# Performance work log

Hardware: AMD Instinct MI355X
Metric: run time of the kernel (lower is better)

Reference implementation:

```python
import jax, jax.numpy as jnp
import numpy as np

BLOCK_SIZE = 4
TOPK = 16
ALPHA = 10.0
EPS = 1e-3


def setup_inputs() -> dict:
    key = jax.random.key(0)
    ks = jax.random.split(key, 5)
    B, H, W, C = 16, 96, 96, 512
    src = jax.random.normal(ks[0], (B, H, W, C), dtype=jnp.float32)
    # torch nn.Linear(C, 64): weight (64, C), bias (64)
    Wq = jax.random.normal(ks[1], (64, C), dtype=jnp.float32) * (C ** -0.5)
    bq = jax.random.normal(ks[2], (64,), dtype=jnp.float32) * 0.01
    Wk = jax.random.normal(ks[3], (64, C), dtype=jnp.float32) * (C ** -0.5)
    bk = jax.random.normal(ks[4], (64,), dtype=jnp.float32) * 0.01
    return {"src": src, "Wq": Wq, "bq": bq, "Wk": Wk, "bk": bk}


def reference(src, Wq, bq, Wk, bk):
    """Faithful JAX version of Zipformer2Encoder.get_select_weight_index.

    Returns (indexes, weights): both (B, num_block_tot, TOPK).
    Balancer is identity at inference (it only shapes gradients in training).
    """
    B, H, W, C = src.shape
    bs = BLOCK_SIZE
    nbh, nbw = H // bs, W // bs
    nb = nbh * nbw          # num_block_tot
    HW = H * W

    # block-mean pooling -> (B, nb, C)
    blocks = src.reshape(B, nbh, bs, nbw, bs, C)
    block_emb = blocks.mean(axis=(2, 4)).reshape(B, nb, C)

    q = block_emb @ Wq.T + bq                      # (B, nb, 64)
    k = src.reshape(B, HW, C) @ Wk.T + bk          # (B, HW, 64)
    scores = jnp.einsum("bnd,bpd->bnp", q, k)      # (B, nb, HW)

    # mask each block's own positions with -inf
    hh = jnp.arange(H) // bs
    ww = jnp.arange(W) // bs
    bid = (hh[:, None] * nbw + ww[None, :]).reshape(HW)        # block id per pixel
    mask = bid[None, :] == jnp.arange(nb)[:, None]             # (nb, HW)
    scores = jnp.where(mask[None], -jnp.inf, scores)

    # descending sort; only the top 2*TOPK entries are ever used
    sscores, indexes = jax.lax.top_k(scores, 2 * TOPK)          # (B, nb, 2*TOPK)

    # (B, nb, TOPK, 2*TOPK)
    diffs = sscores[..., :TOPK, None] - sscores[..., None, :]
    diffs_rms = jnp.sqrt(jnp.mean(diffs ** 2, axis=(1, 2, 3), keepdims=True))
    diffs = diffs * (ALPHA / (diffs_rms + EPS))
    weights = jnp.tanh(jax.nn.sigmoid(diffs).sum(-1) - TOPK)    # (B, nb, TOPK)

    return indexes[..., :TOPK], weights
```

## Files before the change

kernel.cpp:

```cpp
#include <hip/hip_runtime.h>
#include <hip/hip_bf16.h>
#include <math.h>

constexpr int B    = 16;
constexpr int H    = 96;
constexpr int W    = 96;
constexpr int C    = 512;
constexpr int D    = 64;
constexpr int NBH  = 24;
constexpr int NB   = 576;
constexpr int HW   = 9216;
constexpr int TOPK = 16;
constexpr int TK2  = 32;
constexpr int NCAND = 40;
constexpr int CAP  = 64;

typedef __attribute__((ext_vector_type(8))) short bf16x8;
typedef __attribute__((ext_vector_type(4))) float f32x4;

__device__ inline unsigned short f2bf(float x) {
    unsigned int u = __float_as_uint(x);
    return (unsigned short)((u + 0x7FFFu + ((u >> 16) & 1u)) >> 16);
}

__global__ void k_transpose(const float* __restrict__ Wk, const float* __restrict__ Wq,
                            float* __restrict__ WkT, float* __restrict__ WqT) {
    int idx = blockIdx.x * 256 + threadIdx.x;
    if (idx < C * D) {
        int c = idx >> 6, d = idx & 63;
        WkT[c * D + d] = Wk[d * C + c];
        WqT[c * D + d] = Wq[d * C + c];
    }
}

__global__ __launch_bounds__(256, 4) void k_embed(
    const float* __restrict__ src,
    const float* __restrict__ WkT, const float* __restrict__ bk,
    float* __restrict__ k32, float* __restrict__ emb) {
    __shared__ float sS[16][C];

    int t   = threadIdx.x;
    int blk = blockIdx.x;
    int b = blk / NB, n = blk % NB;
    int nh = n / NBH, nw = n % NBH;
    int y0 = nh * 4, x0 = nw * 4;

    #pragma unroll
    for (int r = 0; r < 8; ++r) {
        int f4 = r * 256 + t;
        int px = f4 >> 7, c4 = f4 & 127;
        int dy = px >> 2, dx = px & 3;
        ((float4*)sS[px])[c4] =
            *(const float4*)&src[((size_t)(b * H + y0 + dy) * W + (x0 + dx)) * C + c4 * 4];
    }
    __syncthreads();

    #pragma unroll
    for (int s = 0; s < 2; ++s) {
        int cc = s * 256 + t;
        float sum = sS[0][cc];
        #pragma unroll
        for (int px = 1; px < 16; ++px) sum += sS[px][cc];
        emb[((size_t)b * NB + n) * C + cc] = sum * 0.0625f;
    }

    int d = t & 63, pg = t >> 6;
    const float* s0 = sS[pg * 4 + 0];
    const float* s1 = sS[pg * 4 + 1];
    const float* s2 = sS[pg * 4 + 2];
    const float* s3 = sS[pg * 4 + 3];

    float a0 = 0.f, a1 = 0.f, a2 = 0.f, a3 = 0.f;
    float e0 = 0.f, e1 = 0.f, e2 = 0.f, e3 = 0.f;

    #pragma unroll 2
    for (int cg = 0; cg < 96; ++cg) {
        float4 x0v = *(const float4*)&s0[cg * 4];
        float4 x1v = *(const float4*)&s1[cg * 4];
        float4 x2v = *(const float4*)&s2[cg * 4];
        float4 x3v = *(const float4*)&s3[cg * 4];
        float w0 = WkT[(cg * 4 + 0) * D + d];
        float w1 = WkT[(cg * 4 + 1) * D + d];
        float w2 = WkT[(cg * 4 + 2) * D + d];
        float w3 = WkT[(cg * 4 + 3) * D + d];
        const float* x0f = (const float*)&x0v;
        const float* x1f = (const float*)&x1v;
        const float* x2f = (const float*)&x2v;
        const float* x3f = (const float*)&x3v;
        float wj[4] = {w0, w1, w2, w3};
        #pragma unroll
        for (int j = 0; j < 4; ++j) {
            a0 = __builtin_fmaf(x0f[j], wj[j], a0);
            a1 = __builtin_fmaf(x1f[j], wj[j], a1);
            a2 = __builtin_fmaf(x2f[j], wj[j], a2);
            a3 = __builtin_fmaf(x3f[j], wj[j], a3);
        }
    }
    #pragma unroll 2
    for (int cg = 96; cg < 128; ++cg) {
        float4 x0v = *(const float4*)&s0[cg * 4];
        float4 x1v = *(const float4*)&s1[cg * 4];
        float4 x2v = *(const float4*)&s2[cg * 4];
        float4 x3v = *(const float4*)&s3[cg * 4];
        float w0 = WkT[(cg * 4 + 0) * D + d];
        float w1 = WkT[(cg * 4 + 1) * D + d];
        float w2 = WkT[(cg * 4 + 2) * D + d];
        float w3 = WkT[(cg * 4 + 3) * D + d];
        const float* x0f = (const float*)&x0v;
        const float* x1f = (const float*)&x1v;
        const float* x2f = (const float*)&x2v;
        const float* x3f = (const float*)&x3v;
        float wj[4] = {w0, w1, w2, w3};
        #pragma unroll
        for (int j = 0; j < 4; ++j) {
            e0 = __builtin_fmaf(x0f[j], wj[j], e0);
            e1 = __builtin_fmaf(x1f[j], wj[j], e1);
            e2 = __builtin_fmaf(x2f[j], wj[j], e2);
            e3 = __builtin_fmaf(x3f[j], wj[j], e3);
        }
    }

    float bkd = bk[d];
    #pragma unroll
    for (int u = 0; u < 4; ++u) {
        int pxx = pg * 4 + u;
        int dy = pxx >> 2, dx = pxx & 3;
        size_t p = (size_t)(y0 + dy) * W + (x0 + dx);
        float a = (u == 0 ? a0 : u == 1 ? a1 : u == 2 ? a2 : a3);
        float e = (u == 0 ? e0 : u == 1 ? e1 : u == 2 ? e2 : e3);
        k32[((size_t)b * HW + p) * D + d] = (a + e) + bkd;
    }
}

__global__ __launch_bounds__(256) void k_q(
    const float* __restrict__ emb, const float* __restrict__ WqT,
    const float* __restrict__ bq, float* __restrict__ q32) {
    int t  = threadIdx.x;
    int d  = t & 63;
    int ng = t >> 6;
    int r0 = blockIdx.x * 16 + ng * 4;
    const float* e0 = emb + (size_t)(r0 + 0) * C;
    const float* e1 = emb + (size_t)(r0 + 1) * C;
    const float* e2 = emb + (size_t)(r0 + 2) * C;
    const float* e3 = emb + (size_t)(r0 + 3) * C;

    float qa0 = 0.f, qa1 = 0.f, qa2 = 0.f, qa3 = 0.f;
    float qe0 = 0.f, qe1 = 0.f, qe2 = 0.f, qe3 = 0.f;
    #pragma unroll 2
    for (int cg = 0; cg < 96; ++cg) {
        float4 v0 = *(const float4*)&e0[cg * 4];
        float4 v1 = *(const float4*)&e1[cg * 4];
        float4 v2 = *(const float4*)&e2[cg * 4];
        float4 v3 = *(const float4*)&e3[cg * 4];
        float w0 = WqT[(cg * 4 + 0) * D + d];
        float w1 = WqT[(cg * 4 + 1) * D + d];
        float w2 = WqT[(cg * 4 + 2) * D + d];
        float w3 = WqT[(cg * 4 + 3) * D + d];
        const float* f0 = (const float*)&v0;
        const float* f1 = (const float*)&v1;
        const float* f2 = (const float*)&v2;
        const float* f3 = (const float*)&v3;
        float wj[4] = {w0, w1, w2, w3};
        #pragma unroll
        for (int j = 0; j < 4; ++j) {
            qa0 = __builtin_fmaf(f0[j], wj[j], qa0);
            qa1 = __builtin_fmaf(f1[j], wj[j], qa1);
            qa2 = __builtin_fmaf(f2[j], wj[j], qa2);
            qa3 = __builtin_fmaf(f3[j], wj[j], qa3);
        }
    }
    #pragma unroll 2
    for (int cg = 96; cg < 128; ++cg) {
        float4 v0 = *(const float4*)&e0[cg * 4];
        float4 v1 = *(const float4*)&e1[cg * 4];
        float4 v2 = *(const float4*)&e2[cg * 4];
        float4 v3 = *(const float4*)&e3[cg * 4];
        float w0 = WqT[(cg * 4 + 0) * D + d];
        float w1 = WqT[(cg * 4 + 1) * D + d];
        float w2 = WqT[(cg * 4 + 2) * D + d];
        float w3 = WqT[(cg * 4 + 3) * D + d];
        const float* f0 = (const float*)&v0;
        const float* f1 = (const float*)&v1;
        const float* f2 = (const float*)&v2;
        const float* f3 = (const float*)&v3;
        float wj[4] = {w0, w1, w2, w3};
        #pragma unroll
        for (int j = 0; j < 4; ++j) {
            qe0 = __builtin_fmaf(f0[j], wj[j], qe0);
            qe1 = __builtin_fmaf(f1[j], wj[j], qe1);
            qe2 = __builtin_fmaf(f2[j], wj[j], qe2);
            qe3 = __builtin_fmaf(f3[j], wj[j], qe3);
        }
    }
    float bqd = bq[d];
    q32[(size_t)(r0 + 0) * D + d] = (qa0 + qe0) + bqd;
    q32[(size_t)(r0 + 1) * D + d] = (qa1 + qe1) + bqd;
    q32[(size_t)(r0 + 2) * D + d] = (qa2 + qe2) + bqd;
    q32[(size_t)(r0 + 3) * D + d] = (qa3 + qe3) + bqd;
}

__global__ __launch_bounds__(256, 4) void k_scores(
    const float* __restrict__ q32, const float* __restrict__ k32,
    _Float16* __restrict__ S16) {
    __shared__ unsigned short sQ[64 * 72];
    __shared__ unsigned short sK[64 * 72];
    __shared__ unsigned short sOut[4][16 * 72];

    int t  = threadIdx.x;
    int p0 = blockIdx.x * 64;
    int n0 = blockIdx.y * 64;
    int b  = blockIdx.z;

    const float* qb = q32 + ((size_t)b * NB + n0) * D;
    const float* kb = k32 + ((size_t)b * HW + p0) * D;

    #pragma unroll
    for (int r = 0; r < 4; ++r) {
        int L = r * 256 + t;
        int row = L >> 4, c4 = L & 15;
        float4 vq = *(const float4*)&qb[(size_t)row * D + c4 * 4];
        float4 vk = *(const float4*)&kb[(size_t)row * D + c4 * 4];
        ushort4 hq, hk;
        hq.x = f2bf(vq.x); hq.y = f2bf(vq.y); hq.z = f2bf(vq.z); hq.w = f2bf(vq.w);
        hk.x = f2bf(vk.x); hk.y = f2bf(vk.y); hk.z = f2bf(vk.z); hk.w = f2bf(vk.w);
        *(ushort4*)&sQ[row * 72 + c4 * 4] = hq;
        *(ushort4*)&sK[row * 72 + c4 * 4] = hk;
    }
    __syncthreads();

    int w = t >> 6, l = t & 63;
    int fr = l & 15;
    int kb8 = (l >> 4) * 8;

    f32x4 acc[4] = {f32x4{0,0,0,0}, f32x4{0,0,0,0}, f32x4{0,0,0,0}, f32x4{0,0,0,0}};
    #pragma unroll
    for (int ks = 0; ks < 2; ++ks) {
        bf16x8 a = *(const bf16x8*)&sQ[(16 * w + fr) * 72 + ks * 32 + kb8];
        #pragma unroll
        for (int f = 0; f < 4; ++f) {
            bf16x8 bb = *(const bf16x8*)&sK[(16 * f + fr) * 72 + ks * 32 + kb8];
            acc[f] = __builtin_amdgcn_mfma_f32_16x16x32_bf16(a, bb, acc[f], 0, 0, 0);
        }
    }

    unsigned short* so = &sOut[w][0];
    #pragma unroll
    for (int f = 0; f < 4; ++f)
        #pragma unroll
        for (int r = 0; r < 4; ++r) {
            _Float16 h = (_Float16)acc[f][r];
            so[((l >> 4) * 4 + r) * 72 + 16 * f + (l & 15)] = *(unsigned short*)&h;
        }
    __syncthreads();

    _Float16* Sb = S16 + (size_t)b * NB * HW;
    int orow = l >> 2, oc = (l & 3) * 16;
    uint4 v0 = *(const uint4*)&sOut[w][orow * 72 + oc];
    uint4 v1 = *(const uint4*)&sOut[w][orow * 72 + oc + 8];
    size_t base = (size_t)(n0 + 16 * w + orow) * HW + (p0 + oc);
    *(uint4*)&Sb[base]     = v0;
    *(uint4*)&Sb[base + 8] = v1;
}

__global__ __launch_bounds__(256) void k_topk(
    const _Float16* __restrict__ S16,
    const float* __restrict__ q32, const float* __restrict__ k32,
    int* __restrict__ cidx, float* __restrict__ cval, double* __restrict__ rowss) {
    __shared__ int    hist[4][256];
    __shared__ int    sfx[256];
    __shared__ int    b0s, mAbove, thrS, gcnt;
    __shared__ int    cps[CAP];
    __shared__ float  cv[CAP];
    __shared__ int    cp[CAP];
    __shared__ float  sv[CAP];
    __shared__ int    sp[CAP];
    __shared__ double ssq[TOPK];

    int t   = threadIdx.x;
    int row = blockIdx.x;
    int b = row / NB, n = row % NB;
    int wid = t >> 6;

    #pragma unroll
    for (int w = 0; w < 4; ++w) hist[w][t] = 0;
    if (t == 0) gcnt = 0;
    __syncthreads();

    const unsigned short* Srow = (const unsigned short*)(S16 + (size_t)row * HW);
    unsigned int my[36];
    #pragma unroll
    for (int c = 0; c < 9; ++c) {
        ushort4 v4 = ((const ushort4*)Srow)[c * 256 + t];
        #pragma unroll
        for (int j = 0; j < 4; ++j) {
            unsigned int h = (j == 0 ? v4.x : j == 1 ? v4.y : j == 2 ? v4.z : v4.w);
            unsigned int m = (h & 0x8000u) ? (h ^ 0xFFFFu) : (h | 0x8000u);
            int p = (c * 256 + t) * 4 + j;
            int hh = p / W, ww = p - hh * W;
            if (((hh >> 2) * NBH + (ww >> 2)) == n) m = 0;
            my[c * 4 + j] = m;
            atomicAdd(&hist[wid][m >> 8], 1);
        }
    }
    __syncthreads();

    sfx[t] = hist[0][t] + hist[1][t] + hist[2][t] + hist[3][t];
    __syncthreads();
    #pragma unroll
    for (int off = 1; off < 256; off <<= 1) {
        int v = (t + off < 256) ? sfx[t + off] : 0;
        __syncthreads();
        sfx[t] += v;
        __syncthreads();
    }
    if (sfx[t] >= NCAND && (t == 255 || sfx[t + 1] < NCAND)) {
        b0s = t; mAbove = (t == 255) ? 0 : sfx[t + 1];
    }
    __syncthreads();
    int b0 = b0s, mab = mAbove;
    __syncthreads();

    #pragma unroll
    for (int w = 0; w < 4; ++w) hist[w][t] = 0;
    __syncthreads();
    #pragma unroll
    for (int i = 0; i < 36; ++i)
        if ((int)(my[i] >> 8) == b0) atomicAdd(&hist[wid][my[i] & 255u], 1);
    __syncthreads();
    sfx[t] = hist[0][t] + hist[1][t] + hist[2][t] + hist[3][t];
    __syncthreads();
    #pragma unroll
    for (int off = 1; off < 256; off <<= 1) {
        int v = (t + off < 256) ? sfx[t + off] : 0;
        __syncthreads();
        sfx[t] += v;
        __syncthreads();
    }
    if (mab + sfx[t] >= NCAND && (t == 255 || mab + sfx[t + 1] < NCAND))
        thrS = (b0 << 8) | t;
    __syncthreads();
    unsigned int thr = (unsigned int)thrS;

    #pragma unroll
    for (int i = 0; i < 36; ++i) {
        if (my[i] >= thr) {
            int pos = atomicAdd(&gcnt, 1);
            if (pos < CAP) {
                int c = i >> 2, j = i & 3;
                cps[pos] = (c * 256 + t) * 4 + j;
            }
        }
    }
    __syncthreads();
    int M = min(gcnt, CAP);

    if (t < M) {
        #pragma clang fp contract(off)
        int p = cps[t];
        const float* qr = q32 + (size_t)row * D;
        const float* kr = k32 + ((size_t)b * HW + p) * D;
        float L0 = 0.f, L1 = 0.f, L2 = 0.f, L3 = 0.f;
        #pragma unroll
        for (int j = 0; j < 16; ++j) {
            L0 = L0 + qr[4 * j + 0] * kr[4 * j + 0];
            L1 = L1 + qr[4 * j + 1] * kr[4 * j + 1];
            L2 = L2 + qr[4 * j + 2] * kr[4 * j + 2];
            L3 = L3 + qr[4 * j + 3] * kr[4 * j + 3];
        }
        cv[t] = (L0 + L1) + (L2 + L3);
        cp[t] = p;
    }
    __syncthreads();

    if (t < M) {
        float v = cv[t]; int p = cp[t];
        int rank = 0;
        for (int j = 0; j < M; ++j) {
            float vj = cv[j];
            rank += (vj > v) || (vj == v && cp[j] < p);
        }
        sv[rank] = v; sp[rank] = p;
    }
    __syncthreads();

    if (t < TK2) {
        cval[(size_t)row * TK2 + t] = sv[t];
        cidx[(size_t)row * TK2 + t] = sp[t];
    }
    if (t < TOPK) {
        double vi = (double)sv[t], s = 0.0;
        #pragma unroll
        for (int j = 0; j < TK2; ++j) { double dd = vi - (double)sv[j]; s += dd * dd; }
        ssq[t] = s;
    }
    __syncthreads();
    if (t == 0) {
        double s = 0.0;
        #pragma unroll
        for (int i = 0; i < TOPK; ++i) s += ssq[i];
        rowss[row] = s;
    }
}

__global__ void k_rms(const double* __restrict__ rowss, double* __restrict__ scale) {
    __shared__ double sb[256];
    int b = blockIdx.x, t = threadIdx.x;
    double s = 0.0;
    for (int r = t; r < NB; r += 256) s += rowss[b * NB + r];
    sb[t] = s; __syncthreads();
    for (int st = 128; st > 0; st >>= 1) {
        if (t < st) sb[t] += sb[t + st];
        __syncthreads();
    }
    if (t == 0) {
        double rms = sqrt(sb[0] / ((double)NB * TOPK * TK2));
        scale[b] = 10.0 / (rms + 1e-3);
    }
}

__global__ __launch_bounds__(256) void k_final(
    const int* __restrict__ cidx, const float* __restrict__ cval,
    const double* __restrict__ scale, float* __restrict__ out) {
    __shared__ double sv[16][TK2];
    int t = threadIdx.x;
    int row0 = blockIdx.x * 16;
    for (int idx = t; idx < 16 * TK2; idx += 256) {
        int r = idx >> 5, j = idx & 31;
        sv[r][j] = (double)cval[(size_t)(row0 + r) * TK2 + j];
    }
    __syncthreads();
    int r = t >> 4, i = t & 15;
    int row = row0 + r;
    double scb = scale[row / NB];
    double vi = sv[r][i];
    double s = 0.0;
    #pragma unroll
    for (int j = 0; j < TK2; ++j) {
        double x = (vi - sv[r][j]) * scb;
        s += 1.0 / (1.0 + exp(-x));
    }
    out[(size_t)B * NB * TOPK + (size_t)row * TOPK + i] = (float)tanh(s - (double)TOPK);
    out[(size_t)row * TOPK + i] = (float)cidx[(size_t)row * TK2 + i];
}

__global__ void k_fill(float* out, int nelem) {
    int i = blockIdx.x * 256 + threadIdx.x;
    if (i < nelem) out[i] = -12345.0f;
}

extern "C" void kernel_launch(void* const* d_in, const int* in_sizes, int n_in,
                              void* d_out, int out_size, void* d_ws, size_t ws_size,
                              hipStream_t stream) {
    const float* src = (const float*)d_in[0];
    const float* Wq  = (const float*)d_in[1];
    const float* bq  = (const float*)d_in[2];
    const float* Wk  = (const float*)d_in[3];
    const float* bk  = (const float*)d_in[4];
    float* out = (float*)d_out;

    char* ws = (char*)d_ws;
    size_t oWkT = 0;
    size_t oWqT = oWkT + (size_t)C * D * 4;
    size_t oQ   = oWqT + (size_t)C * D * 4;
    size_t oK   = oQ   + (size_t)B * NB * D * 4;
    size_t oS   = oK   + (size_t)B * HW * D * 4;
    size_t oEmb = oS   + (size_t)B * NB * HW * 2;
    size_t oCV  = oEmb + (size_t)B * NB * C * 4;
    size_t oCI  = oCV  + (size_t)B * NB * TK2 * 4;
    size_t oRS  = oCI  + (size_t)B * NB * TK2 * 4;
    size_t oSc  = oRS  + (size_t)B * NB * 8;
    size_t need = oSc  + (size_t)B * 8;

    if (ws_size < need) {
        k_fill<<<(out_size + 255) / 256, 256, 0, stream>>>(out, out_size);
        return;
    }

    float*     WkT  = (float*)(ws + oWkT);
    float*     WqT  = (float*)(ws + oWqT);
    float*     q32  = (float*)(ws + oQ);
    float*     k32  = (float*)(ws + oK);
    _Float16*  S16  = (_Float16*)(ws + oS);
    float*     emb  = (float*)(ws + oEmb);
    float*     cval = (float*)(ws + oCV);
    int*       cidx = (int*)(ws + oCI);
    double*    rss  = (double*)(ws + oRS);
    double*    scl  = (double*)(ws + oSc);

    k_transpose<<<(C * D + 255) / 256, 256, 0, stream>>>(Wk, Wq, WkT, WqT);
    k_embed<<<B * NB, 256, 0, stream>>>(src, WkT, bk, k32, emb);
    k_q<<<B * NB / 16, 256, 0, stream>>>(emb, WqT, bq, q32);
    k_scores<<<dim3(HW / 64, NB / 64, B), 256, 0, stream>>>(q32, k32, S16);
    k_topk<<<B * NB, 256, 0, stream>>>(S16, q32, k32, cidx, cval, rss);
    k_rms<<<B, 256, 0, stream>>>(rss, scl);
    k_final<<<B * NB / 16, 256, 0, stream>>>(cidx, cval, scl, out);
}
```

Before: 479.7 us.

## Halve embed shared tile, and use privatized histograms with wave-shuffle scans in top-k

k_embed now stages the 16-pixel tile in two 256-channel halves, halving shared memory and raising the launch-bounds occupancy hint from 4 to 8 blocks. The cost is an extra barrier and a second load phase per block. k_topk replaces the per-wave histograms with 8-way privatized copies padded to stride 9, which cuts atomic contention and bank conflicts. It also replaces the barrier-heavy shared-memory suffix scan with wave shuffles plus a per-wave total, and hoists the self-block mask test out of the inner 4-element loop.

Result: no change. 488.2 us (+1.8%).

```diff
diff --git a/kernel.cpp b/kernel.cpp
--- a/kernel.cpp
+++ b/kernel.cpp
@@ -33,11 +33,11 @@
     }
 }
 
-__global__ __launch_bounds__(256, 4) void k_embed(
+__global__ __launch_bounds__(256, 8) void k_embed(
     const float* __restrict__ src,
     const float* __restrict__ WkT, const float* __restrict__ bk,
     float* __restrict__ k32, float* __restrict__ emb) {
-    __shared__ float sS[16][C];
+    __shared__ float sS[16][256];
 
     int t   = threadIdx.x;
     int blk = blockIdx.x;
@@ -45,78 +45,126 @@
     int nh = n / NBH, nw = n % NBH;
     int y0 = nh * 4, x0 = nw * 4;
 
-    #pragma unroll
-    for (int r = 0; r < 8; ++r) {
+    int d = t & 63, pg = t >> 6;
+
+    float a0 = 0.f, a1 = 0.f, a2 = 0.f, a3 = 0.f;
+    float e0 = 0.f, e1 = 0.f, e2 = 0.f, e3 = 0.f;
+
+    #pragma unroll
+    for (int r = 0; r < 4; ++r) {
         int f4 = r * 256 + t;
-        int px = f4 >> 7, c4 = f4 & 127;
+        int px = f4 >> 6, c4 = f4 & 63;
         int dy = px >> 2, dx = px & 3;
         ((float4*)sS[px])[c4] =
             *(const float4*)&src[((size_t)(b * H + y0 + dy) * W + (x0 + dx)) * C + c4 * 4];
     }
     __syncthreads();
 
-    #pragma unroll
-    for (int s = 0; s < 2; ++s) {
-        int cc = s * 256 + t;
-        float sum = sS[0][cc];
-        #pragma unroll
-        for (int px = 1; px < 16; ++px) sum += sS[px][cc];
-        emb[((size_t)b * NB + n) * C + cc] = sum * 0.0625f;
-    }
-
-    int d = t & 63, pg = t >> 6;
-    const float* s0 = sS[pg * 4 + 0];
-    const float* s1 = sS[pg * 4 + 1];
-    const float* s2 = sS[pg * 4 + 2];
-    const float* s3 = sS[pg * 4 + 3];
-
-    float a0 = 0.f, a1 = 0.f, a2 = 0.f, a3 = 0.f;
-    float e0 = 0.f, e1 = 0.f, e2 = 0.f, e3 = 0.f;
-
-    #pragma unroll 2
-    for (int cg = 0; cg < 96; ++cg) {
-        float4 x0v = *(const float4*)&s0[cg * 4];
-        float4 x1v = *(const float4*)&s1[cg * 4];
-        float4 x2v = *(const float4*)&s2[cg * 4];
-        float4 x3v = *(const float4*)&s3[cg * 4];
-        float w0 = WkT[(cg * 4 + 0) * D + d];
-        float w1 = WkT[(cg * 4 + 1) * D + d];
-        float w2 = WkT[(cg * 4 + 2) * D + d];
-        float w3 = WkT[(cg * 4 + 3) * D + d];
-        const float* x0f = (const float*)&x0v;
-        const float* x1f = (const float*)&x1v;
-        const float* x2f = (const float*)&x2v;
-        const float* x3f = (const float*)&x3v;
-        float wj[4] = {w0, w1, w2, w3};
-        #pragma unroll
-        for (int j = 0; j < 4; ++j) {
-            a0 = __builtin_fmaf(x0f[j], wj[j], a0);
-            a1 = __builtin_fmaf(x1f[j], wj[j], a1);
-            a2 = __builtin_fmaf(x2f[j], wj[j], a2);
-            a3 = __builtin_fmaf(x3f[j], wj[j], a3);
-        }
-    }
-    #pragma unroll 2
-    for (int cg = 96; cg < 128; ++cg) {
-        float4 x0v = *(const float4*)&s0[cg * 4];
-        float4 x1v = *(const float4*)&s1[cg * 4];
-        float4 x2v = *(const float4*)&s2[cg * 4];
-        float4 x3v = *(const float4*)&s3[cg * 4];
-        float w0 = WkT[(cg * 4 + 0) * D + d];
-        float w1 = WkT[(cg * 4 + 1) * D + d];
-        float w2 = WkT[(cg * 4 + 2) * D + d];
-        float w3 = WkT[(cg * 4 + 3) * D + d];
-        const float* x0f = (const float*)&x0v;
-        const float* x1f = (const float*)&x1v;
-        const float* x2f = (const float*)&x2v;
-        const float* x3f = (const float*)&x3v;
-        float wj[4] = {w0, w1, w2, w3};
-        #pragma unroll
-        for (int j = 0; j < 4; ++j) {
-            e0 = __builtin_fmaf(x0f[j], wj[j], e0);
-            e1 = __builtin_fmaf(x1f[j], wj[j], e1);
-            e2 = __builtin_fmaf(x2f[j], wj[j], e2);
-            e3 = __builtin_fmaf(x3f[j], wj[j], e3);
+    {
+        float sum = sS[0][t];
+        #pragma unroll
+        for (int px = 1; px < 16; ++px) sum += sS[px][t];
+        emb[((size_t)b * NB + n) * C + t] = sum * 0.0625f;
+    }
+
+    {
+        const float* s0 = sS[pg * 4 + 0];
+        const float* s1 = sS[pg * 4 + 1];
+        const float* s2 = sS[pg * 4 + 2];
+        const float* s3 = sS[pg * 4 + 3];
+        #pragma unroll 2
+        for (int cg = 0; cg < 64; ++cg) {
+            float4 x0v = *(const float4*)&s0[cg * 4];
+            float4 x1v = *(const float4*)&s1[cg * 4];
+            float4 x2v = *(const float4*)&s2[cg * 4];
+            float4 x3v = *(const float4*)&s3[cg * 4];
+            float w0 = WkT[(cg * 4 + 0) * D + d];
+            float w1 = WkT[(cg * 4 + 1) * D + d];
+            float w2 = WkT[(cg * 4 + 2) * D + d];
+            float w3 = WkT[(cg * 4 + 3) * D + d];
+            const float* x0f = (const float*)&x0v;
+            const float* x1f = (const float*)&x1v;
+            const float* x2f = (const float*)&x2v;
+            const float* x3f = (const float*)&x3v;
+            float wj[4] = {w0, w1, w2, w3};
+            #pragma unroll
+            for (int j = 0; j < 4; ++j) {
+                a0 = __builtin_fmaf(x0f[j], wj[j], a0);
+                a1 = __builtin_fmaf(x1f[j], wj[j], a1);
+                a2 = __builtin_fmaf(x2f[j], wj[j], a2);
+                a3 = __builtin_fmaf(x3f[j], wj[j], a3);
+            }
+        }
+    }
+    __syncthreads();
+
+    #pragma unroll
+    for (int r = 0; r < 4; ++r) {
+        int f4 = r * 256 + t;
+        int px = f4 >> 6, c4 = f4 & 63;
+        int dy = px >> 2, dx = px & 3;
+        ((float4*)sS[px])[c4] =
+            *(const float4*)&src[((size_t)(b * H + y0 + dy) * W + (x0 + dx)) * C + 256 + c4 * 4];
+    }
+    __syncthreads();
+
+    {
+        float sum = sS[0][t];
+        #pragma unroll
+        for (int px = 1; px < 16; ++px) sum += sS[px][t];
+        emb[((size_t)b * NB + n) * C + 256 + t] = sum * 0.0625f;
+    }
+
+    {
+        const float* s0 = sS[pg * 4 + 0];
+        const float* s1 = sS[pg * 4 + 1];
+        const float* s2 = sS[pg * 4 + 2];
+        const float* s3 = sS[pg * 4 + 3];
+        #pragma unroll 2
+        for (int cg = 0; cg < 32; ++cg) {
+            float4 x0v = *(const float4*)&s0[cg * 4];
+            float4 x1v = *(const float4*)&s1[cg * 4];
+            float4 x2v = *(const float4*)&s2[cg * 4];
+            float4 x3v = *(const float4*)&s3[cg * 4];
+            float w0 = WkT[(256 + cg * 4 + 0) * D + d];
+            float w1 = WkT[(256 + cg * 4 + 1) * D + d];
+            float w2 = WkT[(256 + cg * 4 + 2) * D + d];
+            float w3 = WkT[(256 + cg * 4 + 3) * D + d];
+            const float* x0f = (const float*)&x0v;
+            const float* x1f = (const float*)&x1v;
+            const float* x2f = (const float*)&x2v;
+            const float* x3f = (const float*)&x3v;
+            float wj[4] = {w0, w1, w2, w3};
+            #pragma unroll
+            for (int j = 0; j < 4; ++j) {
+                a0 = __builtin_fmaf(x0f[j], wj[j], a0);
+                a1 = __builtin_fmaf(x1f[j], wj[j], a1);
+                a2 = __builtin_fmaf(x2f[j], wj[j], a2);
+                a3 = __builtin_fmaf(x3f[j], wj[j], a3);
+            }
+        }
+        #pragma unroll 2
+        for (int cg = 32; cg < 64; ++cg) {
+            float4 x0v = *(const float4*)&s0[cg * 4];
+            float4 x1v = *(const float4*)&s1[cg * 4];
+            float4 x2v = *(const float4*)&s2[cg * 4];
+            float4 x3v = *(const float4*)&s3[cg * 4];
+            float w0 = WkT[(256 + cg * 4 + 0) * D + d];
+            float w1 = WkT[(256 + cg * 4 + 1) * D + d];
+            float w2 = WkT[(256 + cg * 4 + 2) * D + d];
+            float w3 = WkT[(256 + cg * 4 + 3) * D + d];
+            const float* x0f = (const float*)&x0v;
+            const float* x1f = (const float*)&x1v;
+            const float* x2f = (const float*)&x2v;
+            const float* x3f = (const float*)&x3v;
+            float wj[4] = {w0, w1, w2, w3};
+            #pragma unroll
+            for (int j = 0; j < 4; ++j) {
+                e0 = __builtin_fmaf(x0f[j], wj[j], e0);
+                e1 = __builtin_fmaf(x1f[j], wj[j], e1);
+                e2 = __builtin_fmaf(x2f[j], wj[j], e2);
+                e3 = __builtin_fmaf(x3f[j], wj[j], e3);
+            }
         }
     }
 
@@ -266,8 +314,9 @@
     const _Float16* __restrict__ S16,
     const float* __restrict__ q32, const float* __restrict__ k32,
     int* __restrict__ cidx, float* __restrict__ cval, double* __restrict__ rowss) {
-    __shared__ int    hist[4][256];
+    __shared__ int    hist2[256][9];
     __shared__ int    sfx[256];
+    __shared__ int    wtot[4];
     __shared__ int    b0s, mAbove, thrS, gcnt;
     __shared__ int    cps[CAP];
     __shared__ float  cv[CAP];
@@ -279,10 +328,11 @@
     int t   = threadIdx.x;
     int row = blockIdx.x;
     int b = row / NB, n = row % NB;
-    int wid = t >> 6;
-
-    #pragma unroll
-    for (int w = 0; w < 4; ++w) hist[w][t] = 0;
+    int l = t & 63, w = t >> 6;
+    int cpy = t & 7;
+
+    #pragma unroll
+    for (int i = 0; i < 9; ++i) hist2[t][i] = 0;
     if (t == 0) gcnt = 0;
     __syncthreads();
 
@@ -291,51 +341,67 @@
     #pragma unroll
     for (int c = 0; c < 9; ++c) {
         ushort4 v4 = ((const ushort4*)Srow)[c * 256 + t];
+        int base = (c * 256 + t) * 4;
+        int hh = base / W, ww = base - hh * W;
+        bool selfb = (((hh >> 2) * NBH + (ww >> 2)) == n);
         #pragma unroll
         for (int j = 0; j < 4; ++j) {
             unsigned int h = (j == 0 ? v4.x : j == 1 ? v4.y : j == 2 ? v4.z : v4.w);
             unsigned int m = (h & 0x8000u) ? (h ^ 0xFFFFu) : (h | 0x8000u);
-            int p = (c * 256 + t) * 4 + j;
-            int hh = p / W, ww = p - hh * W;
-            if (((hh >> 2) * NBH + (ww >> 2)) == n) m = 0;
+            if (selfb) m = 0;
             my[c * 4 + j] = m;
-            atomicAdd(&hist[wid][m >> 8], 1);
-        }
-    }
-    __syncthreads();
-
-    sfx[t] = hist[0][t] + hist[1][t] + hist[2][t] + hist[3][t];
-    __syncthreads();
-    #pragma unroll
-    for (int off = 1; off < 256; off <<= 1) {
-        int v = (t + off < 256) ? sfx[t + off] : 0;
+            atomicAdd(&hist2[m >> 8][cpy], 1);
+        }
+    }
+    __syncthreads();
+
+    {
+        int v = 0;
+        #pragma unroll
+        for (int i = 0; i < 8; ++i) v += hist2[t][i];
+        #pragma unroll
+        for (int off = 1; off < 64; off <<= 1) {
+            int u = __shfl_down(v, off, 64);
+            if (l + off < 64) v += u;
+        }
+        if (l == 0) wtot[w] = v;
         __syncthreads();
-        sfx[t] += v;
-        __syncthreads();
-    }
+        int add = 0;
+        #pragma unroll
+        for (int w2 = 0; w2 < 4; ++w2) if (w2 > w) add += wtot[w2];
+        sfx[t] = v + add;
+    }
+    __syncthreads();
     if (sfx[t] >= NCAND && (t == 255 || sfx[t + 1] < NCAND)) {
         b0s = t; mAbove = (t == 255) ? 0 : sfx[t + 1];
     }
     __syncthreads();
     int b0 = b0s, mab = mAbove;
-    __syncthreads();
-
-    #pragma unroll
-    for (int w = 0; w < 4; ++w) hist[w][t] = 0;
+
+    #pragma unroll
+    for (int i = 0; i < 9; ++i) hist2[t][i] = 0;
     __syncthreads();
     #pragma unroll
     for (int i = 0; i < 36; ++i)
-        if ((int)(my[i] >> 8) == b0) atomicAdd(&hist[wid][my[i] & 255u], 1);
-    __syncthreads();
-    sfx[t] = hist[0][t] + hist[1][t] + hist[2][t] + hist[3][t];
-    __syncthreads();
-    #pragma unroll
-    for (int off = 1; off < 256; off <<= 1) {
-        int v = (t + off < 256) ? sfx[t + off] : 0;
+        if ((int)(my[i] >> 8) == b0) atomicAdd(&hist2[my[i] & 255u][cpy], 1);
+    __syncthreads();
+    {
+        int v = 0;
+        #pragma unroll
+        for (int i = 0; i < 8; ++i) v += hist2[t][i];
+        #pragma unroll
+        for (int off = 1; off < 64; off <<= 1) {
+            int u = __shfl_down(v, off, 64);
+            if (l + off < 64) v += u;
+        }
+        if (l == 0) wtot[w] = v;
         __syncthreads();
-        sfx[t] += v;
-        __syncthreads();
-    }
+        int add = 0;
+        #pragma unroll
+        for (int w2 = 0; w2 < 4; ++w2) if (w2 > w) add += wtot[w2];
+        sfx[t] = v + add;
+    }
+    __syncthreads();
     if (mab + sfx[t] >= NCAND && (t == 255 || mab + sfx[t + 1] < NCAND))
         thrS = (b0 << 8) | t;
     __syncthreads();
```
